# Optimization experiments

Hardware: AMD Instinct MI355X
Metric: run time of the kernel (lower is better)

Reference implementation:

```python
import jax, jax.numpy as jnp
import numpy as np

N, IN_DIM, OUT_DIM, H = 8192, 512, 512, 1
BN_EPS = 1e-5


def _lin(key, fan_in, fan_out):
    k1, k2 = jax.random.split(key)
    b = 1.0 / np.sqrt(fan_in)
    W = jax.random.uniform(k1, (fan_in, fan_out), jnp.float32, -b, b)
    bias = jax.random.uniform(k2, (fan_out,), jnp.float32, -b, b)
    return W, bias


def setup_inputs() -> dict:
    key = jax.random.key(0)
    ks = jax.random.split(key, 12)
    h = jax.random.normal(ks[0], (N, IN_DIM), jnp.float32)
    A = (jax.random.uniform(ks[1], (N, N)) < 0.01).astype(jnp.float32)
    qw, qb = _lin(ks[2], IN_DIM, OUT_DIM * H)
    kw, kb = _lin(ks[3], IN_DIM, OUT_DIM * H)
    vw, vb = _lin(ks[4], IN_DIM, OUT_DIM * H)
    ow, ob = _lin(ks[5], OUT_DIM, OUT_DIM)
    f1w, f1b = _lin(ks[6], OUT_DIM, OUT_DIM * 2)
    f2w, f2b = _lin(ks[7], OUT_DIM * 2, OUT_DIM)
    bn1_g = jax.random.normal(ks[8], (OUT_DIM,)) * 0.1 + 1.0
    bn1_b = jax.random.normal(ks[9], (OUT_DIM,)) * 0.1
    bn1_m = jax.random.normal(ks[10], (OUT_DIM,)) * 0.1
    bn1_v = jax.random.uniform(ks[11], (OUT_DIM,), jnp.float32, 0.5, 1.5)
    ks2 = jax.random.split(jax.random.fold_in(key, 7), 4)
    bn2_g = jax.random.normal(ks2[0], (OUT_DIM,)) * 0.1 + 1.0
    bn2_b = jax.random.normal(ks2[1], (OUT_DIM,)) * 0.1
    bn2_m = jax.random.normal(ks2[2], (OUT_DIM,)) * 0.1
    bn2_v = jax.random.uniform(ks2[3], (OUT_DIM,), jnp.float32, 0.5, 1.5)
    return dict(A=A, h=h, qw=qw, qb=qb, kw=kw, kb=kb, vw=vw, vb=vb,
                ow=ow, ob=ob, f1w=f1w, f1b=f1b, f2w=f2w, f2b=f2b,
                bn1_g=bn1_g, bn1_b=bn1_b, bn1_m=bn1_m, bn1_v=bn1_v,
                bn2_g=bn2_g, bn2_b=bn2_b, bn2_m=bn2_m, bn2_v=bn2_v)


def _bn_eval(x, g, b, m, v):
    return (x - m) * jax.lax.rsqrt(v + BN_EPS) * g + b


def reference(A, h, qw, qb, kw, kb, vw, vb, ow, ob, f1w, f1b, f2w, f2b,
              bn1_g, bn1_b, bn1_m, bn1_v, bn2_g, bn2_b, bn2_m, bn2_v):
    n = h.shape[0]
    scaling = OUT_DIM ** (-0.5)
    # q/k/v: [N, D, H] as in torch reshape of [N, D*H]
    q = (h @ qw + qb).reshape(n, OUT_DIM, H) * scaling
    k = (h @ kw + kb).reshape(n, OUT_DIM, H)
    v = (h @ vw + vb).reshape(n, OUT_DIM, H)
    qh = jnp.transpose(q, (2, 0, 1))          # (H, N, D)
    kh = jnp.transpose(k, (2, 1, 0))          # (H, D, N)
    vh = jnp.transpose(v, (2, 0, 1))          # (H, N, D)
    attn = jnp.einsum('hnd,hdm->hnm', qh, kh) * A[None]   # (H, N, N)
    attn = jax.nn.softmax(attn, axis=0)        # NOTE: softmax over HEAD axis, as in source
    out = jnp.einsum('hnm,hmd->hnd', attn, vh).reshape(n, H * OUT_DIM)
    # GTLayer (eval mode: dropout = identity, BN uses running stats)
    x = out @ ow + ob
    x = x + h                                  # residual
    x = _bn_eval(x, bn1_g, bn1_b, bn1_m, bn1_v)
    h2 = x
    f = jax.nn.relu(x @ f1w + f1b) @ f2w + f2b
    x = h2 + f
    x = _bn_eval(x, bn2_g, bn2_b, bn2_m, bn2_v)
    return x
```

## Files before the change

### kernel.cpp

```cpp
#include <hip/hip_runtime.h>

#define NROWS 8192
#define DIM 512
#define HID 1024
#define BN_EPS 1e-5f

typedef unsigned short ushort_t;
typedef __attribute__((ext_vector_type(8))) __bf16 bf16x8;
typedef __attribute__((ext_vector_type(4))) float f32x4;

union U4 {
    uint4 u;
    bf16x8 b;
    ushort_t s[8];
};

static __device__ __forceinline__ float b2f(ushort_t u) {
    union { float f; unsigned int i; } c;
    c.i = ((unsigned int)u) << 16;
    return c.f;
}

static __device__ __forceinline__ ushort_t f2b(float f) {
    union { float f; unsigned int i; } c;
    c.f = f;
    unsigned int i = c.i;
    unsigned int r = (i + 0x7FFFu + ((i >> 16) & 1u)) >> 16;
    return (ushort_t)r;
}

__global__ void colsum_kernel(const float* __restrict__ h, float* __restrict__ hs) {
    int t = threadIdx.x;
    int col0 = (t & 127) * 4;
    int rsub = t >> 7;
    int row0 = blockIdx.x * 32;
    float acc[4] = {0.f, 0.f, 0.f, 0.f};
    for (int r = 0; r < 16; ++r) {
        int row = row0 + r * 2 + rsub;
        float4 v = *(const float4*)(h + (size_t)row * DIM + col0);
        acc[0] += v.x; acc[1] += v.y; acc[2] += v.z; acc[3] += v.w;
    }
#pragma unroll
    for (int j = 0; j < 4; ++j) atomicAdd(&hs[col0 + j], acc[j]);
}

__global__ void matvec_kernel(const float* __restrict__ xin, const float* __restrict__ W,
                              const float* __restrict__ bvec, float scaleB,
                              float* __restrict__ outv, int ncols) {
    __shared__ float red[8][32];
    int t = threadIdx.x;
    int col = blockIdx.x * 32 + (t & 31);
    int ks = t >> 5;
    float s = 0.f;
    for (int ki = 0; ki < 64; ++ki) {
        int k = ks * 64 + ki;
        s += xin[k] * W[(size_t)k * ncols + col];
    }
    red[ks][t & 31] = s;
    __syncthreads();
    if (ks == 0) {
        float tot = scaleB * bvec[col];
#pragma unroll
        for (int r = 0; r < 8; ++r) tot += red[r][t & 31];
        outv[col] = tot;
    }
}

__global__ void prep_const_kernel(const float* __restrict__ tvec,
                                  const float* g1, const float* b1,
                                  const float* m1, const float* v1,
                                  const float* g2, const float* b2,
                                  const float* m2, const float* v2,
                                  float* __restrict__ p, float* __restrict__ q0,
                                  float* __restrict__ a2v, float* __restrict__ c2v) {
    int d = threadIdx.x;
    float a1 = g1[d] * rsqrtf(v1[d] + BN_EPS);
    float c1 = b1[d] - m1[d] * a1;
    p[d] = a1;
    q0[d] = tvec[d] * a1 + c1;
    float a2 = g2[d] * rsqrtf(v2[d] + BN_EPS);
    a2v[d] = a2;
    c2v[d] = b2[d] - m2[d] * a2;
}

__global__ void scaleT_kernel(const float* __restrict__ in, const float* __restrict__ p,
                              ushort_t* __restrict__ out, int R, int C) {
    __shared__ float tile[32][33];
    int tx = threadIdx.x & 31, ty = threadIdx.x >> 5;
    int bx = blockIdx.x * 32, by = blockIdx.y * 32;
#pragma unroll
    for (int i = 0; i < 32; i += 8)
        tile[ty + i][tx] = in[(size_t)(by + ty + i) * C + bx + tx];
    __syncthreads();
#pragma unroll
    for (int i = 0; i < 32; i += 8)
        out[(size_t)(bx + ty + i) * R + by + tx] = f2b(tile[tx][ty + i] * p[by + tx]);
}

__global__ void transpose_kernel(const float* __restrict__ in, ushort_t* __restrict__ out,
                                 int R, int C) {
    __shared__ float tile[32][33];
    int tx = threadIdx.x & 31, ty = threadIdx.x >> 5;
    int bx = blockIdx.x * 32, by = blockIdx.y * 32;
#pragma unroll
    for (int i = 0; i < 32; i += 8)
        tile[ty + i][tx] = in[(size_t)(by + ty + i) * C + bx + tx];
    __syncthreads();
#pragma unroll
    for (int i = 0; i < 32; i += 8)
        out[(size_t)(bx + ty + i) * R + by + tx] = f2b(tile[tx][ty + i]);
}

__global__ __launch_bounds__(256) void gemm1_kernel(const float* __restrict__ A,
                                                    const ushort_t* __restrict__ BT,
                                                    const float* __restrict__ bias,
                                                    ushort_t* __restrict__ C) {
    const int K = DIM, Nn = HID, BK = 32, LDA = BK + 8;
    __shared__ ushort_t As[128 * LDA];
    __shared__ ushort_t Bs[128 * LDA];
    int tid = threadIdx.x;
    int lane = tid & 63, w = tid >> 6;
    int wm = (w & 1) * 64, wn = (w >> 1) * 64;
    int bm = blockIdx.y * 128, bn = blockIdx.x * 128;

    f32x4 acc[4][4] = {};

    int ra = tid >> 1, kca = (tid & 1) * 16;
    int r0 = tid >> 2, kc0 = (tid & 3) * 8;
    int r1 = r0 + 64;

    for (int k0 = 0; k0 < K; k0 += BK) {
        __syncthreads();
        const float* ap = A + (size_t)(bm + ra) * K + k0 + kca;
        float4 fa = *(const float4*)(ap + 0);
        float4 fb = *(const float4*)(ap + 4);
        float4 fc = *(const float4*)(ap + 8);
        float4 fd = *(const float4*)(ap + 12);
        uint4 b0 = *(const uint4*)(BT + (size_t)(bn + r0) * K + k0 + kc0);
        uint4 b1 = *(const uint4*)(BT + (size_t)(bn + r1) * K + k0 + kc0);
        ushort_t av[16];
        av[0] = f2b(fa.x); av[1] = f2b(fa.y); av[2] = f2b(fa.z); av[3] = f2b(fa.w);
        av[4] = f2b(fb.x); av[5] = f2b(fb.y); av[6] = f2b(fb.z); av[7] = f2b(fb.w);
        av[8] = f2b(fc.x); av[9] = f2b(fc.y); av[10] = f2b(fc.z); av[11] = f2b(fc.w);
        av[12] = f2b(fd.x); av[13] = f2b(fd.y); av[14] = f2b(fd.z); av[15] = f2b(fd.w);
        *(uint4*)(As + ra * LDA + kca) = *(uint4*)(av);
        *(uint4*)(As + ra * LDA + kca + 8) = *(uint4*)(av + 8);
        *(uint4*)(Bs + r0 * LDA + kc0) = b0;
        *(uint4*)(Bs + r1 * LDA + kc0) = b1;
        __syncthreads();

        int koff = (lane >> 4) * 8;
        bf16x8 af[4], bfr[4];
#pragma unroll
        for (int i = 0; i < 4; ++i) {
            U4 t;
            t.u = *(const uint4*)(As + (wm + i * 16 + (lane & 15)) * LDA + koff);
            af[i] = t.b;
        }
#pragma unroll
        for (int j = 0; j < 4; ++j) {
            U4 t;
            t.u = *(const uint4*)(Bs + (wn + j * 16 + (lane & 15)) * LDA + koff);
            bfr[j] = t.b;
        }
#pragma unroll
        for (int i = 0; i < 4; ++i)
#pragma unroll
            for (int j = 0; j < 4; ++j)
                acc[i][j] = __builtin_amdgcn_mfma_f32_16x16x32_bf16(af[i], bfr[j], acc[i][j], 0, 0, 0);
    }

#pragma unroll
    for (int i = 0; i < 4; ++i) {
        int row0 = bm + wm + i * 16 + (lane >> 4) * 4;
#pragma unroll
        for (int j = 0; j < 4; ++j) {
            int col = bn + wn + j * 16 + (lane & 15);
            float bv = bias[col];
#pragma unroll
            for (int r = 0; r < 4; ++r) {
                float v = fmaxf(acc[i][j][r] + bv, 0.f);
                C[(size_t)(row0 + r) * Nn + col] = f2b(v);
            }
        }
    }
}

__global__ __launch_bounds__(256) void gemm2_kernel(const ushort_t* __restrict__ A,
                                                    const ushort_t* __restrict__ BT,
                                                    const float* __restrict__ bias,
                                                    const float* __restrict__ h,
                                                    const float* __restrict__ p,
                                                    const float* __restrict__ q0,
                                                    const float* __restrict__ a2v,
                                                    const float* __restrict__ c2v,
                                                    float* __restrict__ out) {
    const int K = HID, BK = 32, LDA = BK + 8;
    __shared__ ushort_t As[128 * LDA];
    __shared__ ushort_t Bs[64 * LDA];
    int tid = threadIdx.x;
    int lane = tid & 63, w = tid >> 6;
    int wm = (w & 1) * 64, wn = (w >> 1) * 32;
    int bm = blockIdx.y * 128, bn = blockIdx.x * 64;

    f32x4 acc[4][2] = {};

    int r0 = tid >> 2, kc0 = (tid & 3) * 8;
    int r1 = r0 + 64;

    for (int k0 = 0; k0 < K; k0 += BK) {
        __syncthreads();
        uint4 a0 = *(const uint4*)(A + (size_t)(bm + r0) * K + k0 + kc0);
        uint4 a1 = *(const uint4*)(A + (size_t)(bm + r1) * K + k0 + kc0);
        uint4 bb = *(const uint4*)(BT + (size_t)(bn + r0) * K + k0 + kc0);
        *(uint4*)(As + r0 * LDA + kc0) = a0;
        *(uint4*)(As + r1 * LDA + kc0) = a1;
        *(uint4*)(Bs + r0 * LDA + kc0) = bb;
        __syncthreads();

        int koff = (lane >> 4) * 8;
        bf16x8 af[4], bfr[2];
#pragma unroll
        for (int i = 0; i < 4; ++i) {
            U4 t;
            t.u = *(const uint4*)(As + (wm + i * 16 + (lane & 15)) * LDA + koff);
            af[i] = t.b;
        }
#pragma unroll
        for (int j = 0; j < 2; ++j) {
            U4 t;
            t.u = *(const uint4*)(Bs + (wn + j * 16 + (lane & 15)) * LDA + koff);
            bfr[j] = t.b;
        }
#pragma unroll
        for (int i = 0; i < 4; ++i)
#pragma unroll
            for (int j = 0; j < 2; ++j)
                acc[i][j] = __builtin_amdgcn_mfma_f32_16x16x32_bf16(af[i], bfr[j], acc[i][j], 0, 0, 0);
    }

#pragma unroll
    for (int i = 0; i < 4; ++i) {
        int row0 = bm + wm + i * 16 + (lane >> 4) * 4;
#pragma unroll
        for (int j = 0; j < 2; ++j) {
            int col = bn + wn + j * 16 + (lane & 15);
            float bv = bias[col], pp = p[col], qq = q0[col];
            float aa = a2v[col], cc = c2v[col];
#pragma unroll
            for (int r = 0; r < 4; ++r) {
                int row = row0 + r;
                float x1 = h[(size_t)row * DIM + col] * pp + qq;
                out[(size_t)row * DIM + col] = (x1 + acc[i][j][r] + bv) * aa + cc;
            }
        }
    }
}

extern "C" void kernel_launch(void* const* d_in, const int* in_sizes, int n_in,
                              void* d_out, int out_size, void* d_ws, size_t ws_size,
                              hipStream_t stream) {
    const float* h = (const float*)d_in[1];
    const float* vw = (const float*)d_in[6];
    const float* vb = (const float*)d_in[7];
    const float* ow = (const float*)d_in[8];
    const float* ob = (const float*)d_in[9];
    const float* f1w = (const float*)d_in[10];
    const float* f1b = (const float*)d_in[11];
    const float* f2w = (const float*)d_in[12];
    const float* fb2 = (const float*)d_in[13];
    const float* g1 = (const float*)d_in[14];
    const float* b1 = (const float*)d_in[15];
    const float* m1 = (const float*)d_in[16];
    const float* v1 = (const float*)d_in[17];
    const float* g2 = (const float*)d_in[18];
    const float* b2 = (const float*)d_in[19];
    const float* m2 = (const float*)d_in[20];
    const float* v2 = (const float*)d_in[21];
    float* out = (float*)d_out;

    char* ws = (char*)d_ws;
    float* hs = (float*)(ws + 0);
    float* pC = (float*)(ws + 2048);
    float* q0C = (float*)(ws + 4096);
    float* a2C = (float*)(ws + 6144);
    float* c2C = (float*)(ws + 8192);
    float* sBuf = (float*)(ws + 10240);
    float* tBuf = (float*)(ws + 12288);
    float* b1P = (float*)(ws + 16384);
    ushort_t* W1T = (ushort_t*)(ws + 32768);
    ushort_t* W2T = (ushort_t*)(ws + 32768 + 1048576);
    ushort_t* Z = (ushort_t*)(ws + 32768 + 2097152);

    hipMemsetAsync(hs, 0, 512 * sizeof(float), stream);
    colsum_kernel<<<256, 256, 0, stream>>>(h, hs);
    matvec_kernel<<<16, 256, 0, stream>>>(hs, vw, vb, 8192.0f, sBuf, 512);
    matvec_kernel<<<16, 256, 0, stream>>>(sBuf, ow, ob, 1.0f, tBuf, 512);
    prep_const_kernel<<<1, 512, 0, stream>>>(tBuf, g1, b1, m1, v1, g2, b2, m2, v2,
                                             pC, q0C, a2C, c2C);
    matvec_kernel<<<32, 256, 0, stream>>>(q0C, f1w, f1b, 1.0f, b1P, 1024);
    scaleT_kernel<<<dim3(32, 16), 256, 0, stream>>>(f1w, pC, W1T, 512, 1024);
    transpose_kernel<<<dim3(16, 32), 256, 0, stream>>>(f2w, W2T, 1024, 512);
    gemm1_kernel<<<dim3(8, 64), 256, 0, stream>>>(h, W1T, b1P, Z);
    gemm2_kernel<<<dim3(8, 64), 256, 0, stream>>>(Z, W2T, fb2, h, pC, q0C, a2C, c2C, out);
}
```

Measured before the change: 478.7 us.

## Pre-convert h to bf16 in colsum pass and fuse small prep kernels

The column-sum kernel now also writes a bf16 copy of h. gemm1 then loads bf16 A tiles directly instead of reading fp32 and converting on every K-step in all column blocks. The BN constant prep is folded into the b1 matvec and the gemm2 epilogue, and the two weight transpose kernels are merged into one launch, removing two launches and some workspace traffic. gemm2 now reads the residual h from the bf16 copy, which lowers residual precision and adds an 8MB write in the first pass.

```diff
diff --git a/kernel.cpp b/kernel.cpp
--- a/kernel.cpp
+++ b/kernel.cpp
@@ -29,7 +29,8 @@
     return (ushort_t)r;
 }
 
-__global__ void colsum_kernel(const float* __restrict__ h, float* __restrict__ hs) {
+__global__ void colsum_convert_kernel(const float* __restrict__ h, float* __restrict__ hs,
+                                      ushort_t* __restrict__ hB) {
     int t = threadIdx.x;
     int col0 = (t & 127) * 4;
     int rsub = t >> 7;
@@ -39,6 +40,9 @@
         int row = row0 + r * 2 + rsub;
         float4 v = *(const float4*)(h + (size_t)row * DIM + col0);
         acc[0] += v.x; acc[1] += v.y; acc[2] += v.z; acc[3] += v.w;
+        ushort_t bv[4];
+        bv[0] = f2b(v.x); bv[1] = f2b(v.y); bv[2] = f2b(v.z); bv[3] = f2b(v.w);
+        *(uint2*)(hB + (size_t)row * DIM + col0) = *(uint2*)bv;
     }
 #pragma unroll
     for (int j = 0; j < 4; ++j) atomicAdd(&hs[col0 + j], acc[j]);
@@ -66,52 +70,64 @@
     }
 }
 
-__global__ void prep_const_kernel(const float* __restrict__ tvec,
-                                  const float* g1, const float* b1,
-                                  const float* m1, const float* v1,
-                                  const float* g2, const float* b2,
-                                  const float* m2, const float* v2,
-                                  float* __restrict__ p, float* __restrict__ q0,
-                                  float* __restrict__ a2v, float* __restrict__ c2v) {
-    int d = threadIdx.x;
-    float a1 = g1[d] * rsqrtf(v1[d] + BN_EPS);
-    float c1 = b1[d] - m1[d] * a1;
-    p[d] = a1;
-    q0[d] = tvec[d] * a1 + c1;
-    float a2 = g2[d] * rsqrtf(v2[d] + BN_EPS);
-    a2v[d] = a2;
-    c2v[d] = b2[d] - m2[d] * a2;
-}
-
-__global__ void scaleT_kernel(const float* __restrict__ in, const float* __restrict__ p,
-                              ushort_t* __restrict__ out, int R, int C) {
+__global__ void matvec_b1p_kernel(const float* __restrict__ tvec,
+                                  const float* __restrict__ g1, const float* __restrict__ b1,
+                                  const float* __restrict__ m1, const float* __restrict__ v1,
+                                  const float* __restrict__ W, const float* __restrict__ bvec,
+                                  float* __restrict__ outv) {
+    __shared__ float red[8][32];
+    int t = threadIdx.x;
+    int col = blockIdx.x * 32 + (t & 31);
+    int ks = t >> 5;
+    float s = 0.f;
+    for (int ki = 0; ki < 64; ++ki) {
+        int k = ks * 64 + ki;
+        float a1 = g1[k] * rsqrtf(v1[k] + BN_EPS);
+        float q0 = tvec[k] * a1 + (b1[k] - m1[k] * a1);
+        s += q0 * W[(size_t)k * HID + col];
+    }
+    red[ks][t & 31] = s;
+    __syncthreads();
+    if (ks == 0) {
+        float tot = bvec[col];
+#pragma unroll
+        for (int r = 0; r < 8; ++r) tot += red[r][t & 31];
+        outv[col] = tot;
+    }
+}
+
+__global__ void prepw_kernel(const float* __restrict__ f1w,
+                             const float* __restrict__ g1, const float* __restrict__ v1,
+                             const float* __restrict__ f2w,
+                             ushort_t* __restrict__ W1T, ushort_t* __restrict__ W2T) {
     __shared__ float tile[32][33];
     int tx = threadIdx.x & 31, ty = threadIdx.x >> 5;
-    int bx = blockIdx.x * 32, by = blockIdx.y * 32;
-#pragma unroll
-    for (int i = 0; i < 32; i += 8)
-        tile[ty + i][tx] = in[(size_t)(by + ty + i) * C + bx + tx];
-    __syncthreads();
-#pragma unroll
-    for (int i = 0; i < 32; i += 8)
-        out[(size_t)(bx + ty + i) * R + by + tx] = f2b(tile[tx][ty + i] * p[by + tx]);
-}
-
-__global__ void transpose_kernel(const float* __restrict__ in, ushort_t* __restrict__ out,
-                                 int R, int C) {
-    __shared__ float tile[32][33];
-    int tx = threadIdx.x & 31, ty = threadIdx.x >> 5;
-    int bx = blockIdx.x * 32, by = blockIdx.y * 32;
-#pragma unroll
-    for (int i = 0; i < 32; i += 8)
-        tile[ty + i][tx] = in[(size_t)(by + ty + i) * C + bx + tx];
-    __syncthreads();
-#pragma unroll
-    for (int i = 0; i < 32; i += 8)
-        out[(size_t)(bx + ty + i) * R + by + tx] = f2b(tile[tx][ty + i]);
-}
-
-__global__ __launch_bounds__(256) void gemm1_kernel(const float* __restrict__ A,
+    int b = blockIdx.x;
+    if (b < 512) {
+        int bx = (b & 31) * 32, by = (b >> 5) * 32;
+#pragma unroll
+        for (int i = 0; i < 32; i += 8)
+            tile[ty + i][tx] = f1w[(size_t)(by + ty + i) * HID + bx + tx];
+        __syncthreads();
+        int r = by + tx;
+        float a1 = g1[r] * rsqrtf(v1[r] + BN_EPS);
+#pragma unroll
+        for (int i = 0; i < 32; i += 8)
+            W1T[(size_t)(bx + ty + i) * DIM + r] = f2b(tile[tx][ty + i] * a1);
+    } else {
+        int b2 = b - 512;
+        int bx = (b2 & 15) * 32, by = (b2 >> 4) * 32;
+#pragma unroll
+        for (int i = 0; i < 32; i += 8)
+            tile[ty + i][tx] = f2w[(size_t)(by + ty + i) * DIM + bx + tx];
+        __syncthreads();
+#pragma unroll
+        for (int i = 0; i < 32; i += 8)
+            W2T[(size_t)(bx + ty + i) * HID + by + tx] = f2b(tile[tx][ty + i]);
+    }
+}
+
+__global__ __launch_bounds__(256) void gemm1_kernel(const ushort_t* __restrict__ A,
                                                     const ushort_t* __restrict__ BT,
                                                     const float* __restrict__ bias,
                                                     ushort_t* __restrict__ C) {
@@ -125,26 +141,17 @@
 
     f32x4 acc[4][4] = {};
 
-    int ra = tid >> 1, kca = (tid & 1) * 16;
     int r0 = tid >> 2, kc0 = (tid & 3) * 8;
     int r1 = r0 + 64;
 
     for (int k0 = 0; k0 < K; k0 += BK) {
         __syncthreads();
-        const float* ap = A + (size_t)(bm + ra) * K + k0 + kca;
-        float4 fa = *(const float4*)(ap + 0);
-        float4 fb = *(const float4*)(ap + 4);
-        float4 fc = *(const float4*)(ap + 8);
-        float4 fd = *(const float4*)(ap + 12);
+        uint4 a0 = *(const uint4*)(A + (size_t)(bm + r0) * K + k0 + kc0);
+        uint4 a1 = *(const uint4*)(A + (size_t)(bm + r1) * K + k0 + kc0);
         uint4 b0 = *(const uint4*)(BT + (size_t)(bn + r0) * K + k0 + kc0);
         uint4 b1 = *(const uint4*)(BT + (size_t)(bn + r1) * K + k0 + kc0);
-        ushort_t av[16];
-        av[0] = f2b(fa.x); av[1] = f2b(fa.y); av[2] = f2b(fa.z); av[3] = f2b(fa.w);
-        av[4] = f2b(fb.x); av[5] = f2b(fb.y); av[6] = f2b(fb.z); av[7] = f2b(fb.w);
-        av[8] = f2b(fc.x); av[9] = f2b(fc.y); av[10] = f2b(fc.z); av[11] = f2b(fc.w);
-        av[12] = f2b(fd.x); av[13] = f2b(fd.y); av[14] = f2b(fd.z); av[15] = f2b(fd.w);
-        *(uint4*)(As + ra * LDA + kca) = *(uint4*)(av);
-        *(uint4*)(As + ra * LDA + kca + 8) = *(uint4*)(av + 8);
+        *(uint4*)(As + r0 * LDA + kc0) = a0;
+        *(uint4*)(As + r1 * LDA + kc0) = a1;
         *(uint4*)(Bs + r0 * LDA + kc0) = b0;
         *(uint4*)(Bs + r1 * LDA + kc0) = b1;
         __syncthreads();
@@ -189,11 +196,16 @@
 __global__ __launch_bounds__(256) void gemm2_kernel(const ushort_t* __restrict__ A,
                                                     const ushort_t* __restrict__ BT,
                                                     const float* __restrict__ bias,
-                                                    const float* __restrict__ h,
-                                                    const float* __restrict__ p,
-                                                    const float* __restrict__ q0,
-                                                    const float* __restrict__ a2v,
-                                                    const float* __restrict__ c2v,
+                                                    const ushort_t* __restrict__ hB,
+                                                    const float* __restrict__ tvec,
+                                                    const float* __restrict__ g1,
+                                                    const float* __restrict__ b1,
+                                                    const float* __restrict__ m1,
+                                                    const float* __restrict__ v1,
+                                                    const float* __restrict__ g2,
+                                                    const float* __restrict__ b2,
+                                                    const float* __restrict__ m2,
+                                                    const float* __restrict__ v2,
                                                     float* __restrict__ out) {
     const int K = HID, BK = 32, LDA = BK + 8;
     __shared__ ushort_t As[128 * LDA];
@@ -245,13 +257,16 @@
 #pragma unroll
         for (int j = 0; j < 2; ++j) {
             int col = bn + wn + j * 16 + (lane & 15);
-            float bv = bias[col], pp = p[col], qq = q0[col];
-            float aa = a2v[col], cc = c2v[col];
+            float a1c = g1[col] * rsqrtf(v1[col] + BN_EPS);
+            float q0c = tvec[col] * a1c + (b1[col] - m1[col] * a1c);
+            float a2c = g2[col] * rsqrtf(v2[col] + BN_EPS);
+            float c2c = b2[col] - m2[col] * a2c;
+            float bv = bias[col];
 #pragma unroll
             for (int r = 0; r < 4; ++r) {
                 int row = row0 + r;
-                float x1 = h[(size_t)row * DIM + col] * pp + qq;
-                out[(size_t)row * DIM + col] = (x1 + acc[i][j][r] + bv) * aa + cc;
+                float x1 = b2f(hB[(size_t)row * DIM + col]) * a1c + q0c;
+                out[(size_t)row * DIM + col] = (x1 + acc[i][j][r] + bv) * a2c + c2c;
             }
         }
     }
@@ -281,26 +296,21 @@
 
     char* ws = (char*)d_ws;
     float* hs = (float*)(ws + 0);
-    float* pC = (float*)(ws + 2048);
-    float* q0C = (float*)(ws + 4096);
-    float* a2C = (float*)(ws + 6144);
-    float* c2C = (float*)(ws + 8192);
-    float* sBuf = (float*)(ws + 10240);
-    float* tBuf = (float*)(ws + 12288);
+    float* sBuf = (float*)(ws + 4096);
+    float* tBuf = (float*)(ws + 8192);
     float* b1P = (float*)(ws + 16384);
     ushort_t* W1T = (ushort_t*)(ws + 32768);
     ushort_t* W2T = (ushort_t*)(ws + 32768 + 1048576);
     ushort_t* Z = (ushort_t*)(ws + 32768 + 2097152);
+    ushort_t* hB = (ushort_t*)(ws + 32768 + 2097152 + 16777216);
 
     hipMemsetAsync(hs, 0, 512 * sizeof(float), stream);
-    colsum_kernel<<<256, 256, 0, stream>>>(h, hs);
+    colsum_convert_kernel<<<256, 256, 0, stream>>>(h, hs, hB);
     matvec_kernel<<<16, 256, 0, stream>>>(hs, vw, vb, 8192.0f, sBuf, 512);
     matvec_kernel<<<16, 256, 0, stream>>>(sBuf, ow, ob, 1.0f, tBuf, 512);
-    prep_const_kernel<<<1, 512, 0, stream>>>(tBuf, g1, b1, m1, v1, g2, b2, m2, v2,
-                                             pC, q0C, a2C, c2C);
-    matvec_kernel<<<32, 256, 0, stream>>>(q0C, f1w, f1b, 1.0f, b1P, 1024);
-    scaleT_kernel<<<dim3(32, 16), 256, 0, stream>>>(f1w, pC, W1T, 512, 1024);
-    transpose_kernel<<<dim3(16, 32), 256, 0, stream>>>(f2w, W2T, 1024, 512);
-    gemm1_kernel<<<dim3(8, 64), 256, 0, stream>>>(h, W1T, b1P, Z);
-    gemm2_kernel<<<dim3(8, 64), 256, 0, stream>>>(Z, W2T, fb2, h, pC, q0C, a2C, c2C, out);
-}
+    matvec_b1p_kernel<<<32, 256, 0, stream>>>(tBuf, g1, b1, m1, v1, f1w, f1b, b1P);
+    prepw_kernel<<<1024, 256, 0, stream>>>(f1w, g1, v1, f2w, W1T, W2T);
+    gemm1_kernel<<<dim3(8, 64), 256, 0, stream>>>(hB, W1T, b1P, Z);
+    gemm2_kernel<<<dim3(8, 64), 256, 0, stream>>>(Z, W2T, fb2, hB, tBuf,
+                                                  g1, b1, m1, v1, g2, b2, m2, v2, out);
+}
```

New measurement: 471.1 us. No clear change (-1.6%).
